# Kernel optimization log

Hardware: AMD Instinct MI355X
Metric: run time of the kernel (lower is better)

Reference implementation:

```python
import jax, jax.numpy as jnp
import numpy as np

KSIZE = 7      # gaussian kernel size (SecondMomentMatrixLayer default)
SIGMA = 5.0    # gaussian sigma (default)
ALPHA = 0.05   # corner response alpha (CornerResponseLayer default)


def _gaussian_kernel(ksize, sigma):
    ax = np.arange(ksize, dtype=np.float64) - ksize // 2
    g1 = np.exp(-(ax ** 2) / (2.0 * sigma ** 2))
    k2 = np.outer(g1, g1)
    return (k2 / k2.sum()).astype(np.float32)


def setup_inputs() -> dict:
    key = jax.random.key(0)
    x = jax.random.normal(key, (4, 1, 2048, 2048), dtype=jnp.float32)
    # Sobel filters (ImageGradientsLayer): out-channels [Ix, Iy], shape (2,1,3,3)
    sobel_kernel = jnp.array(
        [[[[-1.0, 0.0, 1.0], [-2.0, 0.0, 2.0], [-1.0, 0.0, 1.0]]],
         [[[-1.0, -2.0, -1.0], [0.0, 0.0, 0.0], [1.0, 2.0, 1.0]]]],
        dtype=jnp.float32)
    # Depthwise (groups=3) gaussian kernel, shape (3,1,7,7)
    g = jnp.asarray(_gaussian_kernel(KSIZE, SIGMA))
    gauss_kernel = jnp.tile(g[None, None], (3, 1, 1, 1))
    return {"x": x, "sobel_kernel": sobel_kernel, "gauss_kernel": gauss_kernel}


def _conv(x, k, pad, groups=1):
    # torch Conv2d is cross-correlation; so is lax.conv_general_dilated
    return jax.lax.conv_general_dilated(
        x, k, window_strides=(1, 1), padding=[(pad, pad), (pad, pad)],
        dimension_numbers=("NCHW", "OIHW", "NCHW"), feature_group_count=groups)


def reference(x, sobel_kernel, gauss_kernel):
    # 1) image gradients via Sobel: (N,1,H,W) -> (N,2,H,W)
    grads = _conv(x, sobel_kernel, pad=1)
    Ix, Iy = grads[:, 0], grads[:, 1]
    # 2) channel products: I_xx, I_yy, I_xy -> (N,3,H,W)
    prods = jnp.stack([Ix * Ix, Iy * Iy, Ix * Iy], axis=1)
    # 3) gaussian-weighted second moments (depthwise conv, groups=3)
    S = _conv(prods, gauss_kernel, pad=KSIZE // 2, groups=3)
    Sxx, Syy, Sxy = S[:, 0], S[:, 1], S[:, 2]
    # 4) corner response R = det - alpha * trace^2 -> (N,1,H,W)
    trace = Sxx + Syy
    R = (Sxx * Syy - Sxy * Sxy - ALPHA * trace * trace)[:, None]
    # 5) NMS: global-median threshold, 7x7 stride-1 maxpool, binarize, scale by R
    median = jnp.quantile(R, 0.5, method="lower")  # torch.median = lower median
    thr = jnp.where(R < median, jnp.float32(0.0), R)
    pooled = jax.lax.reduce_window(
        thr, -jnp.inf, jax.lax.max, window_dimensions=(1, 1, 7, 7),
        window_strides=(1, 1, 1, 1),
        padding=[(0, 0), (0, 0), (3, 3), (3, 3)])
    binarized = jnp.where(thr == pooled, jnp.float32(1.0), jnp.float32(0.0))
    return binarized * R
```

## Files before the change

### kernel.cpp

```cpp
#include <hip/hip_runtime.h>
#include <math.h>

constexpr int IMH = 2048, IMW = 2048, NB = 4;
constexpr int NPIX = NB * IMH * IMW;
constexpr unsigned KSEL = 8388607u;

__device__ __forceinline__ unsigned f2u(float f) {
    unsigned b = __float_as_uint(f);
    return (b & 0x80000000u) ? ~b : (b | 0x80000000u);
}

__device__ __forceinline__ void gauss7(float* a) {
    const double g0 = 0.8352702114112720;
    const double g1 = 0.9231163463866358;
    const double g2 = 0.9801986733067553;
    const double s = 2.0 * (g0 + g1 + g2) + 1.0;
    const double inv = 1.0 / s;
    a[0] = a[6] = (float)(g0 * inv);
    a[1] = a[5] = (float)(g1 * inv);
    a[2] = a[4] = (float)(g2 * inv);
    a[3] = (float)inv;
}

__device__ __forceinline__ float2 fmax2(float2 a, float2 b) {
    return make_float2(fmaxf(a.x, b.x), fmaxf(a.y, b.y));
}

__launch_bounds__(512, 6)
__global__ void harris_R(const float* __restrict__ x, float* __restrict__ Rout,
                         unsigned* __restrict__ hist) {
    __shared__ __align__(16) float smem[12768];
    float2* SIXY = (float2*)smem;
    float* SX = smem + 5472;
    float* STH = smem + 5472;
    unsigned* LH = (unsigned*)smem;

    const int tid = threadIdx.x;
    const int tx = tid & 63, ty = tid >> 6;
    const int x0 = blockIdx.x * 64, y0 = blockIdx.y * 32, b = blockIdx.z;
    const float* xb = x + (size_t)b * IMH * IMW;
    const bool interior = (x0 >= 4) && (x0 + 68 <= IMW) && (y0 >= 4) && (y0 + 36 <= IMH);

    if (interior) {
        const float* xp = xb + (size_t)(y0 - 4) * IMW + (x0 - 4);
        for (int i = tid; i < 1440; i += 512) {
            int r = i / 36, c2 = i - r * 36;
            *(float2*)&SX[r * 72 + 2 * c2] = *(const float2*)&xp[(size_t)r * IMW + 2 * c2];
        }
    } else {
        for (int i = tid; i < 2880; i += 512) {
            int r = i / 72, c = i - r * 72;
            int gy = y0 - 4 + r, gx = x0 - 4 + c;
            float v = 0.f;
            if ((unsigned)gy < (unsigned)IMH && (unsigned)gx < (unsigned)IMW)
                v = xb[(size_t)gy * IMW + gx];
            SX[r * 72 + c] = v;
        }
    }
    __syncthreads();

    for (int i = tid; i < 2660; i += 512) {
        int r = i / 70, c = i - r * 70;
        const float* p = SX + r * 72 + c;
        float x00 = p[0], x01 = p[1], x02 = p[2];
        float x10 = p[72], x12 = p[74];
        float x20 = p[144], x21 = p[145], x22 = p[146];
        float ix = (x02 + 2.0f * x12 + x22) - (x00 + 2.0f * x10 + x20);
        float iy = (x20 + 2.0f * x21 + x22) - (x00 + 2.0f * x01 + x02);
        if (!interior) {
            int gy = y0 - 3 + r, gx = x0 - 3 + c;
            if (!((unsigned)gy < (unsigned)IMH && (unsigned)gx < (unsigned)IMW)) {
                ix = 0.f; iy = 0.f;
            }
        }
        SIXY[r * 72 + c] = make_float2(ix, iy);
    }
    __syncthreads();

    float a[7]; gauss7(a);

    for (int i = tid; i < 2432; i += 512) {
        int r = i >> 6, c = i & 63;
        const float2* p = SIXY + r * 72 + c;
        float sxx = 0.f, syy = 0.f, sxy = 0.f;
        #pragma unroll
        for (int d = 0; d < 7; ++d) {
            float2 v = p[d];
            float t = a[d] * v.x;
            sxx += t * v.x;
            sxy += t * v.y;
            syy += (a[d] * v.y) * v.y;
        }
        STH[r * 64 + c] = sxx;
        STH[2432 + r * 64 + c] = syy;
        STH[4864 + r * 64 + c] = sxy;
    }
    __syncthreads();

    for (int i = tid; i < 4096; i += 512) LH[i] = 0u;

    float vxx[10], vyy[10], vxy[10];
    {
        const float* base = STH + (4 * ty) * 64 + tx;
        #pragma unroll
        for (int t = 0; t < 10; ++t) {
            vxx[t] = base[t * 64];
            vyy[t] = base[2432 + t * 64];
            vxy[t] = base[4864 + t * 64];
        }
    }
    float rv[4];
    float* Rb = Rout + (size_t)b * IMH * IMW + (size_t)y0 * IMW + x0;
    #pragma unroll
    for (int j = 0; j < 4; ++j) {
        float sxx = 0.f, syy = 0.f, sxy = 0.f;
        #pragma unroll
        for (int d = 0; d < 7; ++d) {
            sxx += a[d] * vxx[j + d];
            syy += a[d] * vyy[j + d];
            sxy += a[d] * vxy[j + d];
        }
        float tr = sxx + syy;
        float R = sxx * syy - sxy * sxy - 0.05f * tr * tr;
        rv[j] = R;
        Rb[(size_t)(4 * ty + j) * IMW + tx] = R;
    }
    __syncthreads();

    #pragma unroll
    for (int j = 0; j < 4; ++j) atomicAdd(&LH[f2u(rv[j]) >> 20], 1u);
    __syncthreads();

    const unsigned slot = ((blockIdx.z * gridDim.y + blockIdx.y) * gridDim.x + blockIdx.x) & 7u;
    for (int i = tid; i < 4096; i += 512) {
        unsigned c = LH[i];
        if (c) atomicAdd(&hist[i * 8 + slot], c);
    }
}

__global__ void zero_kernel(unsigned* __restrict__ p, int n, int kidx, unsigned kval) {
    int i = blockIdx.x * blockDim.x + threadIdx.x;
    if (i < n) p[i] = (i == kidx) ? kval : 0u;
}

__global__ void hist2_kernel(const float* __restrict__ R, unsigned* __restrict__ hist,
                             const unsigned* __restrict__ sel) {
    __shared__ unsigned lh[4096];
    for (int i = threadIdx.x; i < 4096; i += 256) lh[i] = 0u;
    __syncthreads();
    const unsigned pref = sel[1];
    const float4* R4 = (const float4*)R;
    const int n4 = NPIX / 4;
    for (int i = blockIdx.x * 256 + threadIdx.x; i < n4; i += gridDim.x * 256) {
        float4 v = R4[i];
        unsigned u;
        u = f2u(v.x); if ((u >> 20) == pref) atomicAdd(&lh[(u >> 8) & 0xFFFu], 1u);
        u = f2u(v.y); if ((u >> 20) == pref) atomicAdd(&lh[(u >> 8) & 0xFFFu], 1u);
        u = f2u(v.z); if ((u >> 20) == pref) atomicAdd(&lh[(u >> 8) & 0xFFFu], 1u);
        u = f2u(v.w); if ((u >> 20) == pref) atomicAdd(&lh[(u >> 8) & 0xFFFu], 1u);
    }
    __syncthreads();
    for (int i = threadIdx.x; i < 4096; i += 256) { unsigned c = lh[i]; if (c) atomicAdd(&hist[i], c); }
}

__global__ void hist3_kernel(const float* __restrict__ R, unsigned* __restrict__ hist,
                             const unsigned* __restrict__ sel) {
    __shared__ unsigned lh[256];
    if (threadIdx.x < 256) lh[threadIdx.x] = 0u;
    __syncthreads();
    const unsigned pref = sel[1];
    const float4* R4 = (const float4*)R;
    const int n4 = NPIX / 4;
    for (int i = blockIdx.x * 256 + threadIdx.x; i < n4; i += gridDim.x * 256) {
        float4 v = R4[i];
        unsigned u;
        u = f2u(v.x); if ((u >> 8) == pref) atomicAdd(&lh[u & 0xFFu], 1u);
        u = f2u(v.y); if ((u >> 8) == pref) atomicAdd(&lh[u & 0xFFu], 1u);
        u = f2u(v.z); if ((u >> 8) == pref) atomicAdd(&lh[u & 0xFFu], 1u);
        u = f2u(v.w); if ((u >> 8) == pref) atomicAdd(&lh[u & 0xFFu], 1u);
    }
    __syncthreads();
    { unsigned c = lh[threadIdx.x]; if (c) atomicAdd(&hist[threadIdx.x], c); }
}

__global__ void select_kernel(const unsigned* __restrict__ hist, unsigned* __restrict__ sel,
                              int bpt, int bits, int final_stage, int slots) {
    __shared__ unsigned part[256];
    __shared__ unsigned grp[16];
    __shared__ int chs;
    __shared__ unsigned runs;
    const int t = threadIdx.x;
    const unsigned krem = sel[0];
    unsigned s = 0;
    for (int i = 0; i < bpt; ++i) {
        unsigned bsum = 0;
        for (int j = 0; j < slots; ++j) bsum += hist[(t * bpt + i) * slots + j];
        s += bsum;
    }
    part[t] = s;
    __syncthreads();
    #pragma unroll
    for (int off = 1; off < 256; off <<= 1) {
        unsigned add = (t >= off) ? part[t - off] : 0u;
        __syncthreads();
        part[t] += add;
        __syncthreads();
    }
    unsigned incl = part[t];
    unsigned excl = incl - s;
    if (excl <= krem && krem < incl) { chs = t; runs = excl; }
    __syncthreads();
    int ch = chs;
    if (t < bpt) {
        unsigned g = 0;
        for (int j = 0; j < slots; ++j) g += hist[(ch * bpt + t) * slots + j];
        grp[t] = g;
    }
    __syncthreads();
    if (t == 0) {
        unsigned r2 = runs; int bsel = ch * bpt;
        for (int j = 0; j < bpt; ++j) {
            unsigned h = grp[j];
            if (r2 + h > krem) { bsel = ch * bpt + j; break; }
            r2 += h;
        }
        sel[0] = krem - r2;
        unsigned pref = (sel[1] << bits) | (unsigned)bsel;
        sel[1] = pref;
        if (final_stage) {
            unsigned fb = (pref & 0x80000000u) ? (pref ^ 0x80000000u) : ~pref;
            ((float*)sel)[2] = __uint_as_float(fb);
        }
    }
}

__launch_bounds__(512, 6)
__global__ void harris_out(const float* __restrict__ R, const unsigned* __restrict__ sel,
                           float* __restrict__ out) {
    __shared__ __align__(16) float smem2[9520];
    float* SR = smem2;
    float2* SM2 = (float2*)(smem2 + 5040);
    const float med = ((const float*)sel)[2];
    const int tid = threadIdx.x;
    const int x0 = blockIdx.x * 64, y0 = blockIdx.y * 64, b = blockIdx.z;
    const float* Rb = R + (size_t)b * IMH * IMW;

    for (int i = tid; i < 70 * 70; i += 512) {
        int r = i / 70, c = i - r * 70;
        int gy = y0 - 3 + r, gx = x0 - 3 + c;
        float v = -INFINITY;
        if ((unsigned)gy < (unsigned)IMH && (unsigned)gx < (unsigned)IMW)
            v = Rb[(size_t)gy * IMW + gx];
        SR[r * 72 + c] = v;
    }
    __syncthreads();

    for (int i = tid; i < 70 * 32; i += 512) {
        int r = i >> 5, p = i & 31;
        const float2* u = (const float2*)(SR + r * 72 + 2 * p);
        float2 u0 = u[0], u1 = u[1], u2 = u[2], u3 = u[3];
        float cv[8] = {u0.x, u0.y, u1.x, u1.y, u2.x, u2.y, u3.x, u3.y};
        float tv[8];
        #pragma unroll
        for (int k = 0; k < 8; ++k) {
            float v = cv[k];
            tv[k] = (v < med) ? ((v == -INFINITY) ? -INFINITY : 0.0f) : v;
        }
        float mid = fmaxf(fmaxf(fmaxf(tv[1], tv[2]), fmaxf(tv[3], tv[4])), fmaxf(tv[5], tv[6]));
        SM2[r * 32 + p] = make_float2(fmaxf(tv[0], mid), fmaxf(tv[7], mid));
    }
    __syncthreads();

    const int p = tid & 31, g = tid >> 5;
    float2 vm[10];
    #pragma unroll
    for (int t = 0; t < 10; ++t) vm[t] = SM2[(4 * g + t) * 32 + p];
    float2 m2[9];
    #pragma unroll
    for (int i = 0; i < 9; ++i) m2[i] = fmax2(vm[i], vm[i + 1]);
    float2 m4[7];
    #pragma unroll
    for (int i = 0; i < 7; ++i) m4[i] = fmax2(m2[i], m2[i + 2]);
    float* ob = out + (size_t)b * IMH * IMW + (size_t)y0 * IMW + x0;
    #pragma unroll
    for (int j = 0; j < 4; ++j) {
        float2 pooled = fmax2(m4[j], m4[j + 3]);
        float vA = SR[(4 * g + j + 3) * 72 + 2 * p + 3];
        float vB = SR[(4 * g + j + 3) * 72 + 2 * p + 4];
        float tA = (vA < med) ? 0.0f : vA;
        float tB = (vB < med) ? 0.0f : vB;
        float2 o = make_float2((tA == pooled.x) ? vA : 0.0f, (tB == pooled.y) ? vB : 0.0f);
        *(float2*)&ob[(size_t)(4 * g + j) * IMW + 2 * p] = o;
    }
}

extern "C" void kernel_launch(void* const* d_in, const int* in_sizes, int n_in,
                              void* d_out, int out_size, void* d_ws, size_t ws_size,
                              hipStream_t stream) {
    const float* x = (const float*)d_in[0];
    float* out = (float*)d_out;

    const size_t needed = (size_t)NPIX * 4 + (32768 + 4096 + 256 + 8) * 4;
    if (ws_size < needed) return;
    float* R = (float*)d_ws;
    unsigned* hbase = (unsigned*)((char*)d_ws + (size_t)NPIX * 4);
    unsigned* h1 = hbase;
    unsigned* h2 = hbase + 32768;
    unsigned* h3 = hbase + 36864;
    unsigned* sel = hbase + 37120;

    zero_kernel<<<(37128 + 255) / 256, 256, 0, stream>>>(hbase, 37128, 37120, KSEL);

    dim3 rgrid(IMW / 64, IMH / 32, NB);
    harris_R<<<rgrid, 512, 0, stream>>>(x, R, h1);

    select_kernel<<<1, 256, 0, stream>>>(h1, sel, 16, 12, 0, 8);
    hist2_kernel<<<2048, 256, 0, stream>>>(R, h2, sel);
    select_kernel<<<1, 256, 0, stream>>>(h2, sel, 16, 12, 0, 1);
    hist3_kernel<<<2048, 256, 0, stream>>>(R, h3, sel);
    select_kernel<<<1, 256, 0, stream>>>(h3, sel, 1, 8, 1, 1);

    dim3 ogrid(IMW / 64, IMH / 64, NB);
    harris_out<<<ogrid, 512, 0, stream>>>(R, sel, out);
}
```

Baseline: 302.0 us.

## Fuse Sobel and horizontal blur in registers, rebalance radix-select histogram bits

Sobel gradients and the horizontal Gaussian pass are now computed together per thread over a 4-wide strip held in registers, which removes the SIXY shared buffer and one block barrier. The smaller shared footprint allows a higher occupancy hint, and the interior tile load switches to float4. The radix-select split changes from 12/12/8 to 11/12/9 bits, which shrinks the first-pass histogram and its global atomics. The histogram passes also read two float4 per iteration. The risks are higher register pressure from the unrolled strips and a larger third-stage histogram.

```diff
diff --git a/kernel.cpp b/kernel.cpp
--- a/kernel.cpp
+++ b/kernel.cpp
@@ -26,14 +26,62 @@
     return make_float2(fmaxf(a.x, b.x), fmaxf(a.y, b.y));
 }
 
-__launch_bounds__(512, 6)
+template<bool CHK>
+__device__ __forceinline__ void hblur_fused(const float* SX, float* STH, const float* a,
+                                            int r, int g, int x0, int y0) {
+    const float* p0 = SX + r * 72 + 4 * g;
+    const float* p1 = p0 + 72;
+    const float* p2 = p1 + 72;
+    float4 A0 = *(const float4*)(p0), B0 = *(const float4*)(p0 + 4), C0 = *(const float4*)(p0 + 8);
+    float4 A1 = *(const float4*)(p1), B1 = *(const float4*)(p1 + 4), C1 = *(const float4*)(p1 + 8);
+    float4 A2 = *(const float4*)(p2), B2 = *(const float4*)(p2 + 4), C2 = *(const float4*)(p2 + 8);
+    float w0[12] = {A0.x, A0.y, A0.z, A0.w, B0.x, B0.y, B0.z, B0.w, C0.x, C0.y, C0.z, C0.w};
+    float w1[12] = {A1.x, A1.y, A1.z, A1.w, B1.x, B1.y, B1.z, B1.w, C1.x, C1.y, C1.z, C1.w};
+    float w2[12] = {A2.x, A2.y, A2.z, A2.w, B2.x, B2.y, B2.z, B2.w, C2.x, C2.y, C2.z, C2.w};
+
+    float cS[12];
+    #pragma unroll
+    for (int j = 0; j < 12; ++j) cS[j] = w0[j] + 2.0f * w1[j] + w2[j];
+    float ix[10], iy[10];
+    #pragma unroll
+    for (int j = 0; j < 10; ++j) {
+        ix[j] = cS[j + 2] - cS[j];
+        float rS2 = w2[j] + 2.0f * w2[j + 1] + w2[j + 2];
+        float rS0 = w0[j] + 2.0f * w0[j + 1] + w0[j + 2];
+        iy[j] = rS2 - rS0;
+        if (CHK) {
+            int gy = y0 - 3 + r, gx = x0 - 3 + (4 * g + j);
+            if (!((unsigned)gy < (unsigned)IMH && (unsigned)gx < (unsigned)IMW)) {
+                ix[j] = 0.f; iy[j] = 0.f;
+            }
+        }
+    }
+    float sxx[4], syy[4], sxy[4];
+    #pragma unroll
+    for (int k = 0; k < 4; ++k) {
+        float xx = 0.f, yy = 0.f, xy = 0.f;
+        #pragma unroll
+        for (int d = 0; d < 7; ++d) {
+            float vx = ix[k + d], vy = iy[k + d];
+            float t = a[d] * vx;
+            xx += t * vx;
+            xy += t * vy;
+            yy += (a[d] * vy) * vy;
+        }
+        sxx[k] = xx; syy[k] = yy; sxy[k] = xy;
+    }
+    *(float4*)&STH[r * 64 + 4 * g]        = make_float4(sxx[0], sxx[1], sxx[2], sxx[3]);
+    *(float4*)&STH[2432 + r * 64 + 4 * g] = make_float4(syy[0], syy[1], syy[2], syy[3]);
+    *(float4*)&STH[4864 + r * 64 + 4 * g] = make_float4(sxy[0], sxy[1], sxy[2], sxy[3]);
+}
+
+__launch_bounds__(512, 8)
 __global__ void harris_R(const float* __restrict__ x, float* __restrict__ Rout,
                          unsigned* __restrict__ hist) {
-    __shared__ __align__(16) float smem[12768];
-    float2* SIXY = (float2*)smem;
-    float* SX = smem + 5472;
-    float* STH = smem + 5472;
-    unsigned* LH = (unsigned*)smem;
+    __shared__ __align__(16) float smem[10176];
+    float* STH = smem;
+    float* SX = smem + 7296;
+    unsigned* LH = (unsigned*)(smem + 7296);
 
     const int tid = threadIdx.x;
     const int tx = tid & 63, ty = tid >> 6;
@@ -43,9 +91,15 @@
 
     if (interior) {
         const float* xp = xb + (size_t)(y0 - 4) * IMW + (x0 - 4);
-        for (int i = tid; i < 1440; i += 512) {
-            int r = i / 36, c2 = i - r * 36;
-            *(float2*)&SX[r * 72 + 2 * c2] = *(const float2*)&xp[(size_t)r * IMW + 2 * c2];
+        int r = tid >> 4, k = tid & 15;
+        *(float4*)&SX[r * 72 + 4 * k] = *(const float4*)&xp[(size_t)r * IMW + 4 * k];
+        if (tid < 128) {
+            int r2 = 32 + (tid >> 4);
+            *(float4*)&SX[r2 * 72 + 4 * k] = *(const float4*)&xp[(size_t)r2 * IMW + 4 * k];
+        }
+        if (tid < 80) {
+            int r3 = tid >> 1, k3 = 16 + (tid & 1);
+            *(float4*)&SX[r3 * 72 + 4 * k3] = *(const float4*)&xp[(size_t)r3 * IMW + 4 * k3];
         }
     } else {
         for (int i = tid; i < 2880; i += 512) {
@@ -59,45 +113,18 @@
     }
     __syncthreads();
 
-    for (int i = tid; i < 2660; i += 512) {
-        int r = i / 70, c = i - r * 70;
-        const float* p = SX + r * 72 + c;
-        float x00 = p[0], x01 = p[1], x02 = p[2];
-        float x10 = p[72], x12 = p[74];
-        float x20 = p[144], x21 = p[145], x22 = p[146];
-        float ix = (x02 + 2.0f * x12 + x22) - (x00 + 2.0f * x10 + x20);
-        float iy = (x20 + 2.0f * x21 + x22) - (x00 + 2.0f * x01 + x02);
-        if (!interior) {
-            int gy = y0 - 3 + r, gx = x0 - 3 + c;
-            if (!((unsigned)gy < (unsigned)IMH && (unsigned)gx < (unsigned)IMW)) {
-                ix = 0.f; iy = 0.f;
-            }
-        }
-        SIXY[r * 72 + c] = make_float2(ix, iy);
-    }
-    __syncthreads();
-
     float a[7]; gauss7(a);
 
-    for (int i = tid; i < 2432; i += 512) {
-        int r = i >> 6, c = i & 63;
-        const float2* p = SIXY + r * 72 + c;
-        float sxx = 0.f, syy = 0.f, sxy = 0.f;
-        #pragma unroll
-        for (int d = 0; d < 7; ++d) {
-            float2 v = p[d];
-            float t = a[d] * v.x;
-            sxx += t * v.x;
-            sxy += t * v.y;
-            syy += (a[d] * v.y) * v.y;
-        }
-        STH[r * 64 + c] = sxx;
-        STH[2432 + r * 64 + c] = syy;
-        STH[4864 + r * 64 + c] = sxy;
-    }
-    __syncthreads();
-
-    for (int i = tid; i < 4096; i += 512) LH[i] = 0u;
+    if (interior) {
+        { int r = tid >> 4, g = tid & 15; hblur_fused<false>(SX, STH, a, r, g, x0, y0); }
+        if (tid < 96) { int r = 32 + (tid >> 4), g = tid & 15; hblur_fused<false>(SX, STH, a, r, g, x0, y0); }
+    } else {
+        { int r = tid >> 4, g = tid & 15; hblur_fused<true>(SX, STH, a, r, g, x0, y0); }
+        if (tid < 96) { int r = 32 + (tid >> 4), g = tid & 15; hblur_fused<true>(SX, STH, a, r, g, x0, y0); }
+    }
+    __syncthreads();
+
+    for (int i = tid; i < 2048; i += 512) LH[i] = 0u;
 
     float vxx[10], vyy[10], vxy[10];
     {
@@ -128,11 +155,11 @@
     __syncthreads();
 
     #pragma unroll
-    for (int j = 0; j < 4; ++j) atomicAdd(&LH[f2u(rv[j]) >> 20], 1u);
+    for (int j = 0; j < 4; ++j) atomicAdd(&LH[f2u(rv[j]) >> 21], 1u);
     __syncthreads();
 
     const unsigned slot = ((blockIdx.z * gridDim.y + blockIdx.y) * gridDim.x + blockIdx.x) & 7u;
-    for (int i = tid; i < 4096; i += 512) {
+    for (int i = tid; i < 2048; i += 512) {
         unsigned c = LH[i];
         if (c) atomicAdd(&hist[i * 8 + slot], c);
     }
@@ -151,13 +178,18 @@
     const unsigned pref = sel[1];
     const float4* R4 = (const float4*)R;
     const int n4 = NPIX / 4;
-    for (int i = blockIdx.x * 256 + threadIdx.x; i < n4; i += gridDim.x * 256) {
-        float4 v = R4[i];
+    for (int i = (blockIdx.x * 256 + threadIdx.x) * 2; i < n4; i += gridDim.x * 512) {
+        float4 v0 = R4[i];
+        float4 v1 = R4[i + 1];
         unsigned u;
-        u = f2u(v.x); if ((u >> 20) == pref) atomicAdd(&lh[(u >> 8) & 0xFFFu], 1u);
-        u = f2u(v.y); if ((u >> 20) == pref) atomicAdd(&lh[(u >> 8) & 0xFFFu], 1u);
-        u = f2u(v.z); if ((u >> 20) == pref) atomicAdd(&lh[(u >> 8) & 0xFFFu], 1u);
-        u = f2u(v.w); if ((u >> 20) == pref) atomicAdd(&lh[(u >> 8) & 0xFFFu], 1u);
+        u = f2u(v0.x); if ((u >> 21) == pref) atomicAdd(&lh[(u >> 9) & 0xFFFu], 1u);
+        u = f2u(v0.y); if ((u >> 21) == pref) atomicAdd(&lh[(u >> 9) & 0xFFFu], 1u);
+        u = f2u(v0.z); if ((u >> 21) == pref) atomicAdd(&lh[(u >> 9) & 0xFFFu], 1u);
+        u = f2u(v0.w); if ((u >> 21) == pref) atomicAdd(&lh[(u >> 9) & 0xFFFu], 1u);
+        u = f2u(v1.x); if ((u >> 21) == pref) atomicAdd(&lh[(u >> 9) & 0xFFFu], 1u);
+        u = f2u(v1.y); if ((u >> 21) == pref) atomicAdd(&lh[(u >> 9) & 0xFFFu], 1u);
+        u = f2u(v1.z); if ((u >> 21) == pref) atomicAdd(&lh[(u >> 9) & 0xFFFu], 1u);
+        u = f2u(v1.w); if ((u >> 21) == pref) atomicAdd(&lh[(u >> 9) & 0xFFFu], 1u);
     }
     __syncthreads();
     for (int i = threadIdx.x; i < 4096; i += 256) { unsigned c = lh[i]; if (c) atomicAdd(&hist[i], c); }
@@ -165,22 +197,30 @@
 
 __global__ void hist3_kernel(const float* __restrict__ R, unsigned* __restrict__ hist,
                              const unsigned* __restrict__ sel) {
-    __shared__ unsigned lh[256];
-    if (threadIdx.x < 256) lh[threadIdx.x] = 0u;
+    __shared__ unsigned lh[512];
+    if (threadIdx.x < 256) { lh[threadIdx.x] = 0u; lh[threadIdx.x + 256] = 0u; }
     __syncthreads();
     const unsigned pref = sel[1];
     const float4* R4 = (const float4*)R;
     const int n4 = NPIX / 4;
-    for (int i = blockIdx.x * 256 + threadIdx.x; i < n4; i += gridDim.x * 256) {
-        float4 v = R4[i];
+    for (int i = (blockIdx.x * 256 + threadIdx.x) * 2; i < n4; i += gridDim.x * 512) {
+        float4 v0 = R4[i];
+        float4 v1 = R4[i + 1];
         unsigned u;
-        u = f2u(v.x); if ((u >> 8) == pref) atomicAdd(&lh[u & 0xFFu], 1u);
-        u = f2u(v.y); if ((u >> 8) == pref) atomicAdd(&lh[u & 0xFFu], 1u);
-        u = f2u(v.z); if ((u >> 8) == pref) atomicAdd(&lh[u & 0xFFu], 1u);
-        u = f2u(v.w); if ((u >> 8) == pref) atomicAdd(&lh[u & 0xFFu], 1u);
-    }
-    __syncthreads();
-    { unsigned c = lh[threadIdx.x]; if (c) atomicAdd(&hist[threadIdx.x], c); }
+        u = f2u(v0.x); if ((u >> 9) == pref) atomicAdd(&lh[u & 0x1FFu], 1u);
+        u = f2u(v0.y); if ((u >> 9) == pref) atomicAdd(&lh[u & 0x1FFu], 1u);
+        u = f2u(v0.z); if ((u >> 9) == pref) atomicAdd(&lh[u & 0x1FFu], 1u);
+        u = f2u(v0.w); if ((u >> 9) == pref) atomicAdd(&lh[u & 0x1FFu], 1u);
+        u = f2u(v1.x); if ((u >> 9) == pref) atomicAdd(&lh[u & 0x1FFu], 1u);
+        u = f2u(v1.y); if ((u >> 9) == pref) atomicAdd(&lh[u & 0x1FFu], 1u);
+        u = f2u(v1.z); if ((u >> 9) == pref) atomicAdd(&lh[u & 0x1FFu], 1u);
+        u = f2u(v1.w); if ((u >> 9) == pref) atomicAdd(&lh[u & 0x1FFu], 1u);
+    }
+    __syncthreads();
+    if (threadIdx.x < 256) {
+        unsigned c = lh[threadIdx.x]; if (c) atomicAdd(&hist[threadIdx.x], c);
+        c = lh[threadIdx.x + 256]; if (c) atomicAdd(&hist[threadIdx.x + 256], c);
+    }
 }
 
 __global__ void select_kernel(const unsigned* __restrict__ hist, unsigned* __restrict__ sel,
@@ -300,25 +340,25 @@
     const float* x = (const float*)d_in[0];
     float* out = (float*)d_out;
 
-    const size_t needed = (size_t)NPIX * 4 + (32768 + 4096 + 256 + 8) * 4;
+    const size_t needed = (size_t)NPIX * 4 + (16384 + 4096 + 512 + 8) * 4;
     if (ws_size < needed) return;
     float* R = (float*)d_ws;
     unsigned* hbase = (unsigned*)((char*)d_ws + (size_t)NPIX * 4);
     unsigned* h1 = hbase;
-    unsigned* h2 = hbase + 32768;
-    unsigned* h3 = hbase + 36864;
-    unsigned* sel = hbase + 37120;
-
-    zero_kernel<<<(37128 + 255) / 256, 256, 0, stream>>>(hbase, 37128, 37120, KSEL);
+    unsigned* h2 = hbase + 16384;
+    unsigned* h3 = hbase + 20480;
+    unsigned* sel = hbase + 20992;
+
+    zero_kernel<<<(21000 + 255) / 256, 256, 0, stream>>>(hbase, 21000, 20992, KSEL);
 
     dim3 rgrid(IMW / 64, IMH / 32, NB);
     harris_R<<<rgrid, 512, 0, stream>>>(x, R, h1);
 
-    select_kernel<<<1, 256, 0, stream>>>(h1, sel, 16, 12, 0, 8);
+    select_kernel<<<1, 256, 0, stream>>>(h1, sel, 8, 11, 0, 8);
     hist2_kernel<<<2048, 256, 0, stream>>>(R, h2, sel);
     select_kernel<<<1, 256, 0, stream>>>(h2, sel, 16, 12, 0, 1);
     hist3_kernel<<<2048, 256, 0, stream>>>(R, h3, sel);
-    select_kernel<<<1, 256, 0, stream>>>(h3, sel, 1, 8, 1, 1);
+    select_kernel<<<1, 256, 0, stream>>>(h3, sel, 2, 9, 1, 1);
 
     dim3 ogrid(IMW / 64, IMH / 64, NB);
     harris_out<<<ogrid, 512, 0, stream>>>(R, sel, out);
```

Result: slower. 443.0 us (+46.7%).
